# Kernel optimization log

Measured on AMD Instinct MI355X. Metric: run time of the kernel, lower is better.

## Reference

```python
import jax, jax.numpy as jnp
import numpy as np

D_STATE = 16
D_CONV = 4
DT_RANK = 64
D_INNER = 2048
CHANNELS = 1024

def silu(x):
    return x * jax.nn.sigmoid(x)

def setup_inputs() -> dict:
    key = jax.random.key(0)
    ks = jax.random.split(key, 12)
    B, C, T = 2, CHANNELS, 1024
    s = 0.02
    return {
        "x": jax.random.normal(ks[0], (B, C, T), jnp.float32),
        "norm_w": jnp.ones((C,), jnp.float32),
        "norm_b": jnp.zeros((C,), jnp.float32),
        "in_proj_w": jax.random.normal(ks[1], (2 * D_INNER, C), jnp.float32) * s,
        "conv_w": jax.random.normal(ks[2], (D_INNER, 1, D_CONV), jnp.float32) * 0.2,
        "conv_b": jnp.zeros((D_INNER,), jnp.float32),
        "x_proj_w": jax.random.normal(ks[3], (DT_RANK + 2 * D_STATE, D_INNER), jnp.float32) * s,
        "dt_proj_w": jax.random.normal(ks[4], (D_INNER, DT_RANK), jnp.float32) * (DT_RANK ** -0.5),
        "dt_proj_b": jax.random.normal(ks[5], (D_INNER,), jnp.float32) * 0.5 - 4.0,
        "A_log": jnp.log(jnp.arange(1, D_STATE + 1, dtype=jnp.float32))[None, :].repeat(D_INNER, 0),
        "D": jnp.ones((D_INNER,), jnp.float32),
        "out_proj_w": jax.random.normal(ks[6], (C, D_INNER), jnp.float32) * s,
    }

def reference(x, norm_w, norm_b, in_proj_w, conv_w, conv_b, x_proj_w,
              dt_proj_w, dt_proj_b, A_log, D, out_proj_w):
    B, C, T = x.shape
    residual = x
    # LayerNorm over channels: [B,T,C]
    xt = jnp.transpose(x, (0, 2, 1))
    mu = jnp.mean(xt, -1, keepdims=True)
    var = jnp.mean(jnp.square(xt - mu), -1, keepdims=True)
    x_n = (xt - mu) * jax.lax.rsqrt(var + 1e-5) * norm_w + norm_b
    # input projection -> x_in, z  [B,T,d_inner]
    xz = x_n @ in_proj_w.T
    x_in, z = jnp.split(xz, 2, axis=-1)
    # causal depthwise conv1d (torch pads d_conv-1 both sides then slices [:T] == left pad)
    xc = jax.lax.conv_general_dilated(
        jnp.transpose(x_in, (0, 2, 1)),  # [B, d_inner, T]
        conv_w,                            # [d_inner, 1, K]
        window_strides=(1,),
        padding=[(D_CONV - 1, 0)],
        feature_group_count=D_INNER,
        dimension_numbers=("NCH", "OIH", "NCH"),
    ) + conv_b[None, :, None]
    x_c = silu(jnp.transpose(xc, (0, 2, 1)))  # [B,T,d_inner]
    # low-rank dt / B / C projections
    x_dbl = x_c @ x_proj_w.T  # [B,T,dt_rank+2*d_state]
    dt_raw = x_dbl[..., :DT_RANK]
    B_seq = x_dbl[..., DT_RANK:DT_RANK + D_STATE]
    C_seq = x_dbl[..., DT_RANK + D_STATE:]
    dt = jax.nn.softplus(dt_raw @ dt_proj_w.T + dt_proj_b)  # [B,T,d_inner]
    A = -jnp.exp(A_log)  # [d_inner, d_state]
    dA = jnp.exp(dt[..., None] * A[None, None])                      # [B,T,di,ds]
    dBu = dt[..., None] * B_seq[:, :, None, :] * x_c[..., None]       # [B,T,di,ds]
    # sequential selective scan over T
    def step(h, inp):
        dA_t, dBu_t, C_t = inp
        h = dA_t * h + dBu_t                     # [B,di,ds]
        y = jnp.sum(h * C_t[:, None, :], -1)     # [B,di]
        return h, y
    h0 = jnp.zeros((B, D_INNER, D_STATE), x.dtype)
    _, ys = jax.lax.scan(
        step, h0,
        (jnp.transpose(dA, (1, 0, 2, 3)), jnp.transpose(dBu, (1, 0, 2, 3)),
         jnp.transpose(C_seq, (1, 0, 2))))
    y_ssm = jnp.transpose(ys, (1, 0, 2)) + D * x_c  # [B,T,di]
    y = y_ssm * silu(z)
    out = jnp.transpose(y @ out_proj_w.T, (0, 2, 1))  # [B,C,T]
    return out + residual
```

## Files before the change

kernel.cpp:

```cpp
#include <hip/hip_runtime.h>
#include <math.h>

#define C_DIM 1024
#define T_DIM 1024
#define DIN 2048
#define NSTATE 16
#define NC 32
#define LCH 32

typedef __attribute__((ext_vector_type(8))) short bf16x8;
typedef __attribute__((ext_vector_type(4))) float f32x4;
typedef unsigned short ushort_t;

__device__ __forceinline__ float sigmoidf_(float x){ return 1.f/(1.f+__expf(-x)); }

__device__ __forceinline__ unsigned short f2bf(float f){
    union { float f; unsigned u; } v; v.f = f;
    unsigned r = v.u + 0x7fff + ((v.u >> 16) & 1);
    return (unsigned short)(r >> 16);
}
__device__ __forceinline__ float bf2f(ushort_t u){
    union { unsigned u; float f; } v; v.u = ((unsigned)u) << 16;
    return v.f;
}

#define GLDS(g, l) __builtin_amdgcn_global_load_lds( \
    (const __attribute__((address_space(1))) void*)(g), \
    (__attribute__((address_space(3))) void*)(l), 16, 0, 0)

__global__ void prep_w(const float* __restrict__ ipw, const float* __restrict__ dpw,
                       const float* __restrict__ xpw, const float* __restrict__ opw,
                       ushort_t* __restrict__ w_in, ushort_t* __restrict__ w_dt,
                       ushort_t* __restrict__ wxp, ushort_t* __restrict__ w_out)
{
    int blk = blockIdx.x, tid = threadIdx.x;
    if (blk < 4096) {
        int i = blk*256 + tid;
        float4 v = ((const float4*)ipw)[i];
        ushort4 o; o.x=f2bf(v.x); o.y=f2bf(v.y); o.z=f2bf(v.z); o.w=f2bf(v.w);
        ((ushort4*)w_in)[i] = o;
    } else if (blk < 4224) {
        int i = (blk-4096)*256 + tid;
        float4 v = ((const float4*)dpw)[i];
        ushort4 o; o.x=f2bf(v.x); o.y=f2bf(v.y); o.z=f2bf(v.z); o.w=f2bf(v.w);
        ((ushort4*)w_dt)[i] = o;
    } else if (blk < 4480) {
        int i = (blk-4224)*256 + tid;
        ushort4 o; o.x=0; o.y=0; o.z=0; o.w=0;
        if (i < 49152) {
            float4 v = ((const float4*)xpw)[i];
            o.x=f2bf(v.x); o.y=f2bf(v.y); o.z=f2bf(v.z); o.w=f2bf(v.w);
        }
        ((ushort4*)wxp)[i] = o;
    } else {
        int i = (blk-4480)*256 + tid;
        float4 v = ((const float4*)opw)[i];
        ushort4 o; o.x=f2bf(v.x); o.y=f2bf(v.y); o.z=f2bf(v.z); o.w=f2bf(v.w);
        ((ushort4*)w_out)[i] = o;
    }
}

__global__ void ln_v2(const float* __restrict__ x, const float* __restrict__ w,
                      const float* __restrict__ bvec, ushort_t* __restrict__ xn)
{
    __shared__ float tile[8*1040];
    int blk = blockIdx.x;
    int b = blk >> 7, t0 = (blk & 127) * 8;
    int tid = threadIdx.x;
    #pragma unroll
    for (int it = 0; it < 8; it++) {
        int idx = tid + it*256;
        int c = idx >> 1, q = idx & 1;
        float4 v = *(const float4*)&x[((size_t)b*C_DIM + c)*T_DIM + t0 + q*4];
        tile[(q*4+0)*1040 + c] = v.x;
        tile[(q*4+1)*1040 + c] = v.y;
        tile[(q*4+2)*1040 + c] = v.z;
        tile[(q*4+3)*1040 + c] = v.w;
    }
    __syncthreads();
    int tg = tid >> 5, k = tid & 31;
    float sum = 0.f, sumsq = 0.f;
    #pragma unroll
    for (int j = 0; j < 32; j++) {
        float v = tile[tg*1040 + k + 32*j];
        sum += v; sumsq += v*v;
    }
    #pragma unroll
    for (int off = 16; off > 0; off >>= 1) {
        sum   += __shfl_xor(sum, off, 32);
        sumsq += __shfl_xor(sumsq, off, 32);
    }
    float mu  = sum * (1.f/1024.f);
    float var = sumsq * (1.f/1024.f) - mu*mu;
    float rstd = rsqrtf(var + 1e-5f);
    size_t orow = ((size_t)b*T_DIM + t0 + tg)*C_DIM;
    #pragma unroll
    for (int j = 0; j < 8; j++) {
        int c = 4*k + 128*j;
        float4 v = *(const float4*)&tile[tg*1040 + c];
        float4 wv = *(const float4*)&w[c];
        float4 bv = *(const float4*)&bvec[c];
        ushort4 o;
        o.x = f2bf((v.x-mu)*rstd*wv.x + bv.x);
        o.y = f2bf((v.y-mu)*rstd*wv.y + bv.y);
        o.z = f2bf((v.z-mu)*rstd*wv.z + bv.z);
        o.w = f2bf((v.w-mu)*rstd*wv.w + bv.w);
        *(ushort4*)&xn[orow + c] = o;
    }
}

__global__ __launch_bounds__(256, 2)
void gemm_mfma(const ushort_t* __restrict__ A, const ushort_t* __restrict__ W,
               const float* __restrict__ bias, void* __restrict__ Co_,
               int M, int N, int Kloop, int lda, int ldw, int mode)
{
    __shared__ __align__(16) ushort_t As[128*32];
    __shared__ __align__(16) ushort_t Ws[128*32];
    int tid  = threadIdx.x;
    int lane = tid & 63, wave = tid >> 6;
    int wm = (wave >> 1) * 64, wn = (wave & 1) * 64;
    int lrow = lane & 15, quad = lane >> 4;
    int m0 = blockIdx.y << 7, n0 = blockIdx.x << 7;
    int srow = lane >> 2, soff = (lane & 3) * 8;
    int kz = blockIdx.z * Kloop;
    A += kz; W += kz;

    f32x4 acc[4][4];
    #pragma unroll
    for (int i = 0; i < 4; i++)
        #pragma unroll
        for (int j = 0; j < 4; j++)
            acc[i][j] = (f32x4){0.f, 0.f, 0.f, 0.f};

    for (int k0 = 0; k0 < Kloop; k0 += 32) {
        #pragma unroll
        for (int h = 0; h < 2; h++) {
            int r = wave*32 + h*16;
            GLDS(&A[(size_t)(m0 + r + srow)*lda + k0 + soff], &As[r*32]);
            GLDS(&W[(size_t)(n0 + r + srow)*ldw + k0 + soff], &Ws[r*32]);
        }
        __syncthreads();
        bf16x8 af[4], bfr[4];
        #pragma unroll
        for (int i = 0; i < 4; i++)
            af[i] = *(const bf16x8*)&As[(wm + i*16 + lrow)*32 + quad*8];
        #pragma unroll
        for (int j = 0; j < 4; j++)
            bfr[j] = *(const bf16x8*)&Ws[(wn + j*16 + lrow)*32 + quad*8];
        #pragma unroll
        for (int i = 0; i < 4; i++)
            #pragma unroll
            for (int j = 0; j < 4; j++)
                acc[i][j] = __builtin_amdgcn_mfma_f32_16x16x32_bf16(af[i], bfr[j], acc[i][j], 0, 0, 0);
        __syncthreads();
    }

    #pragma unroll
    for (int i = 0; i < 4; i++) {
        #pragma unroll
        for (int j = 0; j < 4; j++) {
            int mb = m0 + wm + i*16 + quad*4;
            int n  = n0 + wn + j*16 + lrow;
            if (mode == 1) {
                ushort_t* Co = (ushort_t*)Co_;
                float bv = bias[n];
                #pragma unroll
                for (int r = 0; r < 4; r++) {
                    float v = acc[i][j][r] + bv;
                    v = (v > 15.f) ? v : __logf(1.f + __expf(v));
                    Co[(size_t)(mb + r)*N + n] = f2bf(v);
                }
            } else if (mode == 3) {
                ushort_t* Co = (ushort_t*)Co_;
                #pragma unroll
                for (int r = 0; r < 4; r++)
                    Co[(size_t)(mb + r)*N + n] = f2bf(acc[i][j][r]);
            } else {
                float* Co = (float*)Co_ + (size_t)blockIdx.z * M * N;
                #pragma unroll
                for (int r = 0; r < 4; r++)
                    Co[(size_t)(mb + r)*N + n] = acc[i][j][r];
            }
        }
    }
}

__global__ __launch_bounds__(256, 2)
void gemm_mfma64(const ushort_t* __restrict__ A, const ushort_t* __restrict__ W,
                 const float* __restrict__ resid, float* __restrict__ Co,
                 int M, int N, int K)
{
    __shared__ __align__(16) ushort_t As[64*32];
    __shared__ __align__(16) ushort_t Ws[128*32];
    int tid  = threadIdx.x;
    int lane = tid & 63, wave = tid >> 6;
    int lrow = lane & 15, quad = lane >> 4;
    int m0 = blockIdx.y << 6, n0 = blockIdx.x << 7;
    int srow = lane >> 2, soff = (lane & 3) * 8;

    f32x4 acc[4][2];
    #pragma unroll
    for (int i = 0; i < 4; i++) { acc[i][0] = (f32x4){0,0,0,0}; acc[i][1] = (f32x4){0,0,0,0}; }

    for (int k0 = 0; k0 < K; k0 += 32) {
        GLDS(&A[(size_t)(m0 + wave*16 + srow)*K + k0 + soff], &As[(wave*16)*32]);
        GLDS(&W[(size_t)(n0 + wave*32 + srow)*K + k0 + soff], &Ws[(wave*32)*32]);
        GLDS(&W[(size_t)(n0 + wave*32 + 16 + srow)*K + k0 + soff], &Ws[(wave*32+16)*32]);
        __syncthreads();
        bf16x8 af[4], bfr[2];
        #pragma unroll
        for (int i = 0; i < 4; i++)
            af[i] = *(const bf16x8*)&As[(i*16 + lrow)*32 + quad*8];
        #pragma unroll
        for (int j = 0; j < 2; j++)
            bfr[j] = *(const bf16x8*)&Ws[(wave*32 + j*16 + lrow)*32 + quad*8];
        #pragma unroll
        for (int i = 0; i < 4; i++)
            #pragma unroll
            for (int j = 0; j < 2; j++)
                acc[i][j] = __builtin_amdgcn_mfma_f32_16x16x32_bf16(af[i], bfr[j], acc[i][j], 0, 0, 0);
        __syncthreads();
    }

    #pragma unroll
    for (int i = 0; i < 4; i++) {
        #pragma unroll
        for (int j = 0; j < 2; j++) {
            int mb = m0 + i*16 + quad*4;
            int n  = n0 + wave*32 + j*16 + lrow;
            int b = mb >> 10, tb = mb & 1023;
            size_t oi = ((size_t)b*C_DIM + n)*T_DIM + tb;
            float4 rv = *(const float4*)&resid[oi];
            float4 ov;
            ov.x = acc[i][j][0] + rv.x;
            ov.y = acc[i][j][1] + rv.y;
            ov.z = acc[i][j][2] + rv.z;
            ov.w = acc[i][j][3] + rv.w;
            *(float4*)&Co[oi] = ov;
        }
    }
}

__global__ void reduce_xproj(const float* __restrict__ xpp, float* __restrict__ xdbl,
                             ushort_t* __restrict__ dtA)
{
    int gid = blockIdx.x*256 + threadIdx.x;
    float4 s = {0.f,0.f,0.f,0.f};
    #pragma unroll
    for (int z = 0; z < 8; z++) {
        float4 v = ((const float4*)xpp)[(size_t)z*65536 + gid];
        s.x += v.x; s.y += v.y; s.z += v.z; s.w += v.w;
    }
    ((float4*)xdbl)[gid] = s;
    int c4 = gid & 31;
    if (c4 < 16) {
        int row = gid >> 5;
        ushort4 o;
        o.x = f2bf(s.x); o.y = f2bf(s.y); o.z = f2bf(s.z); o.w = f2bf(s.w);
        ((ushort4*)dtA)[row*16 + c4] = o;
    }
}

__global__ void conv_silu(const ushort_t* __restrict__ xz, const float* __restrict__ cw,
                          const float* __restrict__ cb, ushort_t* __restrict__ xc)
{
    int idx = blockIdx.x*256 + threadIdx.x;
    int d4 = idx & 511;
    int bt = idx >> 9;
    int t  = bt & 1023;
    int d = d4 << 2;
    const ushort_t* base = xz + (size_t)bt*(2*DIN) + d;
    float a0 = cb[d], a1 = cb[d+1], a2 = cb[d+2], a3 = cb[d+3];
    #pragma unroll
    for (int j = 0; j < 4; j++) {
        int tt = t + j - 3;
        if (tt >= 0) {
            ushort4 v = *(const ushort4*)(base + (long)(j-3)*(2*DIN));
            a0 += cw[(d+0)*4+j]*bf2f(v.x);
            a1 += cw[(d+1)*4+j]*bf2f(v.y);
            a2 += cw[(d+2)*4+j]*bf2f(v.z);
            a3 += cw[(d+3)*4+j]*bf2f(v.w);
        }
    }
    ushort4 o;
    o.x = f2bf(a0*sigmoidf_(a0));
    o.y = f2bf(a1*sigmoidf_(a1));
    o.z = f2bf(a2*sigmoidf_(a2));
    o.w = f2bf(a3*sigmoidf_(a3));
    ((ushort4*)xc)[idx] = o;
}

__global__ void scan_p1(const ushort_t* __restrict__ dtb, const ushort_t* __restrict__ xcb,
                        const float* __restrict__ xdbl,
                        float* __restrict__ hpart, float* __restrict__ Ppart)
{
    int d = blockIdx.x*256 + threadIdx.x;
    int c = blockIdx.y, b = blockIdx.z;
    size_t bt0 = (size_t)b*T_DIM + c*LCH;
    __shared__ float BC[LCH][32];
    {
        int r = threadIdx.x >> 3, c4 = threadIdx.x & 7;
        *(float4*)&BC[r][c4*4] = *(const float4*)&xdbl[(bt0 + r)*128 + 64 + c4*4];
    }
    __syncthreads();
    float h[NSTATE];
    #pragma unroll
    for (int s = 0; s < NSTATE; s++) h[s] = 0.f;
    float sumdt = 0.f;
    const ushort_t* dt_p = dtb + bt0*DIN + d;
    const ushort_t* xc_p = xcb + bt0*DIN + d;
    for (int t = 0; t < LCH; t++) {
        float dtv = bf2f(dt_p[(size_t)t*DIN]);
        float xcv = bf2f(xc_p[(size_t)t*DIN]);
        sumdt += dtv;
        float w = __expf(-dtv);
        float u = dtv * xcv;
        float p = 1.f;
        #pragma unroll
        for (int s = 0; s < NSTATE; s++) { p *= w; h[s] = p*h[s] + u*BC[t][s]; }
    }
    float wsum = __expf(-sumdt);
    size_t base = ((size_t)(b*NC + c)*NSTATE)*DIN + d;
    float p = 1.f;
    #pragma unroll
    for (int s = 0; s < NSTATE; s++) {
        p *= wsum;
        hpart[base + (size_t)s*DIN] = h[s];
        Ppart[base + (size_t)s*DIN] = p;
    }
}

__global__ void scan_combine(float* __restrict__ hpart, const float* __restrict__ Ppart)
{
    int gid = blockIdx.x*256 + threadIdx.x;
    int b = gid >> 15;
    int sd = gid & 32767;
    float run = 0.f;
    for (int c = 0; c < NC; c++) {
        size_t oi = ((size_t)(b*NC + c)*NSTATE)*DIN + sd;
        float hp = hpart[oi];
        float Pp = Ppart[oi];
        hpart[oi] = run;
        run = hp + Pp*run;
    }
}

__global__ void scan_p2(const ushort_t* __restrict__ dtb, const ushort_t* __restrict__ xcb,
                        const float* __restrict__ xdbl, const ushort_t* __restrict__ xz,
                        const float* __restrict__ Dp, const float* __restrict__ hinit,
                        ushort_t* __restrict__ y)
{
    int d = blockIdx.x*256 + threadIdx.x;
    int c = blockIdx.y, b = blockIdx.z;
    size_t bt0 = (size_t)b*T_DIM + c*LCH;
    __shared__ float BC[LCH][32];
    {
        int r = threadIdx.x >> 3, c4 = threadIdx.x & 7;
        *(float4*)&BC[r][c4*4] = *(const float4*)&xdbl[(bt0 + r)*128 + 64 + c4*4];
    }
    __syncthreads();
    float h[NSTATE];
    size_t base = ((size_t)(b*NC + c)*NSTATE)*DIN + d;
    #pragma unroll
    for (int s = 0; s < NSTATE; s++) h[s] = hinit[base + (size_t)s*DIN];
    float Dv = Dp[d];
    const ushort_t* dt_p = dtb + bt0*DIN + d;
    const ushort_t* xc_p = xcb + bt0*DIN + d;
    const ushort_t* z_p  = xz + bt0*(2*DIN) + DIN + d;
    ushort_t* y_p = y + bt0*DIN + d;
    for (int t = 0; t < LCH; t++) {
        float dtv = bf2f(dt_p[(size_t)t*DIN]);
        float xcv = bf2f(xc_p[(size_t)t*DIN]);
        float w = __expf(-dtv);
        float u = dtv * xcv;
        float p = 1.f;
        float yv = 0.f;
        #pragma unroll
        for (int s = 0; s < NSTATE; s++) {
            p *= w;
            h[s] = p*h[s] + u*BC[t][s];
            yv += h[s]*BC[t][16+s];
        }
        yv += Dv*xcv;
        float zv = bf2f(z_p[(size_t)t*(2*DIN)]);
        y_p[(size_t)t*DIN] = f2bf(yv * zv * sigmoidf_(zv));
    }
}

extern "C" void kernel_launch(void* const* d_in, const int* in_sizes, int n_in,
                              void* d_out, int out_size, void* d_ws, size_t ws_size,
                              hipStream_t stream)
{
    const float* x         = (const float*)d_in[0];
    const float* norm_w    = (const float*)d_in[1];
    const float* norm_b    = (const float*)d_in[2];
    const float* in_proj_w = (const float*)d_in[3];
    const float* conv_w    = (const float*)d_in[4];
    const float* conv_b    = (const float*)d_in[5];
    const float* x_proj_w  = (const float*)d_in[6];
    const float* dt_proj_w = (const float*)d_in[7];
    const float* dt_proj_b = (const float*)d_in[8];
    const float* A_log     = (const float*)d_in[9];
    const float* Dp        = (const float*)d_in[10];
    const float* out_proj_w= (const float*)d_in[11];
    float* out = (float*)d_out;
    (void)A_log;

    const size_t MB = 1048576;
    char* wsb = (char*)d_ws;
    ushort_t* xz    = (ushort_t*)(wsb);
    ushort_t* xcb   = (ushort_t*)(wsb + 16*MB);
    ushort_t* dtb   = (ushort_t*)(wsb + 24*MB);
    ushort_t* w_in  = dtb;
    float*    xdbl  = (float*)(wsb + 32*MB);
    ushort_t* yb    = (ushort_t*)(wsb + 33*MB);
    ushort_t* xn    = (ushort_t*)(wsb + 41*MB);
    ushort_t* w_dt  = (ushort_t*)(wsb + 45*MB);
    ushort_t* dtA   = (ushort_t*)(wsb + 45*MB + 262144);
    ushort_t* wxp   = (ushort_t*)(wsb + 45*MB + 524288);
    float*    hpart = (float*)(wsb + 46*MB);
    float*    Ppart = (float*)(wsb + 54*MB);
    ushort_t* w_out = (ushort_t*)(wsb + 62*MB);
    float*    xpp   = hpart;

    prep_w<<<6528, 256, 0, stream>>>(in_proj_w, dt_proj_w, x_proj_w, out_proj_w,
                                     w_in, w_dt, wxp, w_out);
    ln_v2<<<256, 256, 0, stream>>>(x, norm_w, norm_b, xn);
    gemm_mfma<<<dim3(32, 16), 256, 0, stream>>>(xn, w_in, nullptr, xz,
                                                2048, 4096, 1024, 1024, 1024, 3);
    conv_silu<<<4096, 256, 0, stream>>>(xz, conv_w, conv_b, xcb);
    gemm_mfma<<<dim3(1, 16, 8), 256, 0, stream>>>(xcb, wxp, nullptr, xpp,
                                                  2048, 128, 256, 2048, 2048, 0);
    reduce_xproj<<<256, 256, 0, stream>>>(xpp, xdbl, dtA);
    gemm_mfma<<<dim3(16, 16), 256, 0, stream>>>(dtA, w_dt, dt_proj_b, dtb,
                                                2048, 2048, 64, 64, 64, 1);
    scan_p1<<<dim3(8, NC, 2), 256, 0, stream>>>(dtb, xcb, xdbl, hpart, Ppart);
    scan_combine<<<256, 256, 0, stream>>>(hpart, Ppart);
    scan_p2<<<dim3(8, NC, 2), 256, 0, stream>>>(dtb, xcb, xdbl, xz, Dp, hpart, yb);
    gemm_mfma64<<<dim3(8, 32), 256, 0, stream>>>(yb, w_out, x, out, 2048, 1024, 2048);
}
```

Baseline: 261.8 us.

## Fuse all stages into one persistent megakernel with global atomic barriers

Replaces the eleven separate kernel launches (weight prep, layernorm, GEMMs, conv, x_proj reduce, scan phases, out_proj) with one persistent 512-block kernel whose stages are separated by software grid barriers built on atomic counters. Weight conversion now runs alongside layernorm in the same stage. This removes per-launch overhead and inter-kernel gaps. In exchange it relies on all 512 blocks being co-resident, which could deadlock otherwise, and some stages use only part of the grid, leaving blocks idle at each barrier.

```diff
diff --git a/kernel.cpp b/kernel.cpp
--- a/kernel.cpp
+++ b/kernel.cpp
@@ -7,6 +7,7 @@
 #define NSTATE 16
 #define NC 32
 #define LCH 32
+#define NBLK 512
 
 typedef __attribute__((ext_vector_type(8))) short bf16x8;
 typedef __attribute__((ext_vector_type(4))) float f32x4;
@@ -28,362 +29,431 @@
     (const __attribute__((address_space(1))) void*)(g), \
     (__attribute__((address_space(3))) void*)(l), 16, 0, 0)
 
-__global__ void prep_w(const float* __restrict__ ipw, const float* __restrict__ dpw,
-                       const float* __restrict__ xpw, const float* __restrict__ opw,
-                       ushort_t* __restrict__ w_in, ushort_t* __restrict__ w_dt,
-                       ushort_t* __restrict__ wxp, ushort_t* __restrict__ w_out)
+#define MB 1048576
+
+__device__ __forceinline__ void gbar(int* cnt, int stage)
 {
+    __syncthreads();
+    if (threadIdx.x == 0) {
+        __threadfence();
+        __hip_atomic_fetch_add(&cnt[stage], 1, __ATOMIC_ACQ_REL, __HIP_MEMORY_SCOPE_AGENT);
+        while (__hip_atomic_load(&cnt[stage], __ATOMIC_ACQUIRE, __HIP_MEMORY_SCOPE_AGENT) < NBLK)
+            __builtin_amdgcn_s_sleep(8);
+        __threadfence();
+    }
+    __syncthreads();
+}
+
+__global__ void init_bar(int* cnt)
+{
+    if (threadIdx.x < 16) cnt[threadIdx.x] = 0;
+}
+
+__global__ __launch_bounds__(256, 2)
+void mamba_mega(const float* __restrict__ x, const float* __restrict__ norm_w,
+                const float* __restrict__ norm_b, const float* __restrict__ ipw,
+                const float* __restrict__ cw, const float* __restrict__ cb,
+                const float* __restrict__ xpw, const float* __restrict__ dpw,
+                const float* __restrict__ dpb, const float* __restrict__ Dp,
+                const float* __restrict__ opw, float* __restrict__ out,
+                char* __restrict__ wsb)
+{
+    ushort_t* xz    = (ushort_t*)(wsb);
+    ushort_t* xcb   = (ushort_t*)(wsb + 16*MB);
+    ushort_t* dtb   = (ushort_t*)(wsb + 24*MB);
+    ushort_t* w_in  = dtb;
+    ushort_t* yb    = (ushort_t*)(wsb + 32*MB);
+    ushort_t* xn    = (ushort_t*)(wsb + 40*MB);
+    ushort_t* w_out = (ushort_t*)(wsb + 44*MB);
+    ushort_t* w_dt  = (ushort_t*)(wsb + 48*MB);
+    ushort_t* dtA   = (ushort_t*)(wsb + 48*MB + 262144);
+    ushort_t* wxp   = (ushort_t*)(wsb + 48*MB + 524288);
+    float*    BCf   = (float*)(wsb + 49*MB);
+    float*    hpart = (float*)(wsb + 50*MB);
+    float*    Ppart = (float*)(wsb + 58*MB);
+    float*    xpp   = (float*)(wsb + 66*MB);
+    int*      bar   = (int*)(wsb + 80*MB);
+
+    __shared__ __align__(16) char smem[33280];
+    float*    lntile = (float*)smem;
+    ushort_t* sm_a   = (ushort_t*)smem;
+    ushort_t* sm_b   = (ushort_t*)(smem + 8192);
+    float (*sBC)[32] = (float(*)[32])(smem + 16384);
+
     int blk = blockIdx.x, tid = threadIdx.x;
-    if (blk < 4096) {
-        int i = blk*256 + tid;
-        float4 v = ((const float4*)ipw)[i];
-        ushort4 o; o.x=f2bf(v.x); o.y=f2bf(v.y); o.z=f2bf(v.z); o.w=f2bf(v.w);
-        ((ushort4*)w_in)[i] = o;
-    } else if (blk < 4224) {
-        int i = (blk-4096)*256 + tid;
-        float4 v = ((const float4*)dpw)[i];
-        ushort4 o; o.x=f2bf(v.x); o.y=f2bf(v.y); o.z=f2bf(v.z); o.w=f2bf(v.w);
-        ((ushort4*)w_dt)[i] = o;
-    } else if (blk < 4480) {
-        int i = (blk-4224)*256 + tid;
-        ushort4 o; o.x=0; o.y=0; o.z=0; o.w=0;
-        if (i < 49152) {
-            float4 v = ((const float4*)xpw)[i];
-            o.x=f2bf(v.x); o.y=f2bf(v.y); o.z=f2bf(v.z); o.w=f2bf(v.w);
-        }
-        ((ushort4*)wxp)[i] = o;
+    int lane = tid & 63, wave = tid >> 6;
+    int lrow = lane & 15, quad = lane >> 4;
+    int srow = lane >> 2, soff = (lane & 3) * 8;
+    int wm = (wave >> 1) * 64, wn = (wave & 1) * 64;
+
+    if (blk < 256) {
+        int b = blk >> 7, t0 = (blk & 127) * 8;
+        #pragma unroll
+        for (int it = 0; it < 8; it++) {
+            int idx = tid + it*256;
+            int c = idx >> 1, q = idx & 1;
+            float4 v = *(const float4*)&x[((size_t)b*C_DIM + c)*T_DIM + t0 + q*4];
+            lntile[(q*4+0)*1040 + c] = v.x;
+            lntile[(q*4+1)*1040 + c] = v.y;
+            lntile[(q*4+2)*1040 + c] = v.z;
+            lntile[(q*4+3)*1040 + c] = v.w;
+        }
+        __syncthreads();
+        int tg = tid >> 5, k = tid & 31;
+        float sum = 0.f, sumsq = 0.f;
+        #pragma unroll
+        for (int j = 0; j < 32; j++) {
+            float v = lntile[tg*1040 + k + 32*j];
+            sum += v; sumsq += v*v;
+        }
+        #pragma unroll
+        for (int off = 16; off > 0; off >>= 1) {
+            sum   += __shfl_xor(sum, off, 32);
+            sumsq += __shfl_xor(sumsq, off, 32);
+        }
+        float mu  = sum * (1.f/1024.f);
+        float var = sumsq * (1.f/1024.f) - mu*mu;
+        float rstd = rsqrtf(var + 1e-5f);
+        size_t orow = ((size_t)b*T_DIM + t0 + tg)*C_DIM;
+        #pragma unroll
+        for (int j = 0; j < 8; j++) {
+            int c = 4*k + 128*j;
+            float4 v = *(const float4*)&lntile[tg*1040 + c];
+            float4 wv = *(const float4*)&norm_w[c];
+            float4 bv = *(const float4*)&norm_b[c];
+            ushort4 o;
+            o.x = f2bf((v.x-mu)*rstd*wv.x + bv.x);
+            o.y = f2bf((v.y-mu)*rstd*wv.y + bv.y);
+            o.z = f2bf((v.z-mu)*rstd*wv.z + bv.z);
+            o.w = f2bf((v.w-mu)*rstd*wv.w + bv.w);
+            *(ushort4*)&xn[orow + c] = o;
+        }
     } else {
-        int i = (blk-4480)*256 + tid;
-        float4 v = ((const float4*)opw)[i];
-        ushort4 o; o.x=f2bf(v.x); o.y=f2bf(v.y); o.z=f2bf(v.z); o.w=f2bf(v.w);
-        ((ushort4*)w_out)[i] = o;
-    }
-}
-
-__global__ void ln_v2(const float* __restrict__ x, const float* __restrict__ w,
-                      const float* __restrict__ bvec, ushort_t* __restrict__ xn)
-{
-    __shared__ float tile[8*1040];
-    int blk = blockIdx.x;
-    int b = blk >> 7, t0 = (blk & 127) * 8;
-    int tid = threadIdx.x;
-    #pragma unroll
-    for (int it = 0; it < 8; it++) {
-        int idx = tid + it*256;
-        int c = idx >> 1, q = idx & 1;
-        float4 v = *(const float4*)&x[((size_t)b*C_DIM + c)*T_DIM + t0 + q*4];
-        tile[(q*4+0)*1040 + c] = v.x;
-        tile[(q*4+1)*1040 + c] = v.y;
-        tile[(q*4+2)*1040 + c] = v.z;
-        tile[(q*4+3)*1040 + c] = v.w;
-    }
-    __syncthreads();
-    int tg = tid >> 5, k = tid & 31;
-    float sum = 0.f, sumsq = 0.f;
-    #pragma unroll
-    for (int j = 0; j < 32; j++) {
-        float v = tile[tg*1040 + k + 32*j];
-        sum += v; sumsq += v*v;
-    }
-    #pragma unroll
-    for (int off = 16; off > 0; off >>= 1) {
-        sum   += __shfl_xor(sum, off, 32);
-        sumsq += __shfl_xor(sumsq, off, 32);
-    }
-    float mu  = sum * (1.f/1024.f);
-    float var = sumsq * (1.f/1024.f) - mu*mu;
-    float rstd = rsqrtf(var + 1e-5f);
-    size_t orow = ((size_t)b*T_DIM + t0 + tg)*C_DIM;
-    #pragma unroll
-    for (int j = 0; j < 8; j++) {
-        int c = 4*k + 128*j;
-        float4 v = *(const float4*)&tile[tg*1040 + c];
-        float4 wv = *(const float4*)&w[c];
-        float4 bv = *(const float4*)&bvec[c];
+        for (int g = (blk-256)*256 + tid; g < 1671168; g += 65536) {
+            if (g < 1048576) {
+                float4 v = ((const float4*)ipw)[g];
+                ushort4 o; o.x=f2bf(v.x); o.y=f2bf(v.y); o.z=f2bf(v.z); o.w=f2bf(v.w);
+                ((ushort4*)w_in)[g] = o;
+            } else if (g < 1081344) {
+                int i = g - 1048576;
+                float4 v = ((const float4*)dpw)[i];
+                ushort4 o; o.x=f2bf(v.x); o.y=f2bf(v.y); o.z=f2bf(v.z); o.w=f2bf(v.w);
+                ((ushort4*)w_dt)[i] = o;
+            } else if (g < 1146880) {
+                int i = g - 1081344;
+                ushort4 o; o.x=0; o.y=0; o.z=0; o.w=0;
+                if (i < 49152) {
+                    float4 v = ((const float4*)xpw)[i];
+                    o.x=f2bf(v.x); o.y=f2bf(v.y); o.z=f2bf(v.z); o.w=f2bf(v.w);
+                }
+                ((ushort4*)wxp)[i] = o;
+            } else {
+                int i = g - 1146880;
+                float4 v = ((const float4*)opw)[i];
+                ushort4 o; o.x=f2bf(v.x); o.y=f2bf(v.y); o.z=f2bf(v.z); o.w=f2bf(v.w);
+                ((ushort4*)w_out)[i] = o;
+            }
+        }
+    }
+    gbar(bar, 0);
+
+    {
+        int m0 = (blk >> 5) << 7, n0 = (blk & 31) << 7;
+        f32x4 acc[4][4];
+        #pragma unroll
+        for (int i = 0; i < 4; i++)
+            #pragma unroll
+            for (int j = 0; j < 4; j++) acc[i][j] = (f32x4){0.f,0.f,0.f,0.f};
+        for (int k0 = 0; k0 < 1024; k0 += 32) {
+            #pragma unroll
+            for (int h = 0; h < 2; h++) {
+                int r = wave*32 + h*16;
+                GLDS(&xn[(size_t)(m0 + r + srow)*1024 + k0 + soff], &sm_a[r*32]);
+                GLDS(&w_in[(size_t)(n0 + r + srow)*1024 + k0 + soff], &sm_b[r*32]);
+            }
+            __syncthreads();
+            bf16x8 af[4], bfr[4];
+            #pragma unroll
+            for (int i = 0; i < 4; i++) af[i] = *(const bf16x8*)&sm_a[(wm + i*16 + lrow)*32 + quad*8];
+            #pragma unroll
+            for (int j = 0; j < 4; j++) bfr[j] = *(const bf16x8*)&sm_b[(wn + j*16 + lrow)*32 + quad*8];
+            #pragma unroll
+            for (int i = 0; i < 4; i++)
+                #pragma unroll
+                for (int j = 0; j < 4; j++)
+                    acc[i][j] = __builtin_amdgcn_mfma_f32_16x16x32_bf16(af[i], bfr[j], acc[i][j], 0, 0, 0);
+            __syncthreads();
+        }
+        #pragma unroll
+        for (int i = 0; i < 4; i++)
+            #pragma unroll
+            for (int j = 0; j < 4; j++) {
+                int mb = m0 + wm + i*16 + quad*4;
+                int n  = n0 + wn + j*16 + lrow;
+                #pragma unroll
+                for (int r = 0; r < 4; r++)
+                    xz[(size_t)(mb + r)*4096 + n] = f2bf(acc[i][j][r]);
+            }
+    }
+    gbar(bar, 1);
+
+    for (int idx = blk*256 + tid; idx < 1048576; idx += 131072) {
+        int d4 = idx & 511;
+        int bt = idx >> 9;
+        int t  = bt & 1023;
+        int d = d4 << 2;
+        const ushort_t* base = xz + (size_t)bt*4096 + d;
+        float a0 = cb[d], a1 = cb[d+1], a2 = cb[d+2], a3 = cb[d+3];
+        #pragma unroll
+        for (int j = 0; j < 4; j++) {
+            int tt = t + j - 3;
+            if (tt >= 0) {
+                ushort4 v = *(const ushort4*)(base + (long)(j-3)*4096);
+                a0 += cw[(d+0)*4+j]*bf2f(v.x);
+                a1 += cw[(d+1)*4+j]*bf2f(v.y);
+                a2 += cw[(d+2)*4+j]*bf2f(v.z);
+                a3 += cw[(d+3)*4+j]*bf2f(v.w);
+            }
+        }
         ushort4 o;
-        o.x = f2bf((v.x-mu)*rstd*wv.x + bv.x);
-        o.y = f2bf((v.y-mu)*rstd*wv.y + bv.y);
-        o.z = f2bf((v.z-mu)*rstd*wv.z + bv.z);
-        o.w = f2bf((v.w-mu)*rstd*wv.w + bv.w);
-        *(ushort4*)&xn[orow + c] = o;
-    }
-}
-
-__global__ __launch_bounds__(256, 2)
-void gemm_mfma(const ushort_t* __restrict__ A, const ushort_t* __restrict__ W,
-               const float* __restrict__ bias, void* __restrict__ Co_,
-               int M, int N, int Kloop, int lda, int ldw, int mode)
-{
-    __shared__ __align__(16) ushort_t As[128*32];
-    __shared__ __align__(16) ushort_t Ws[128*32];
-    int tid  = threadIdx.x;
-    int lane = tid & 63, wave = tid >> 6;
-    int wm = (wave >> 1) * 64, wn = (wave & 1) * 64;
-    int lrow = lane & 15, quad = lane >> 4;
-    int m0 = blockIdx.y << 7, n0 = blockIdx.x << 7;
-    int srow = lane >> 2, soff = (lane & 3) * 8;
-    int kz = blockIdx.z * Kloop;
-    A += kz; W += kz;
-
-    f32x4 acc[4][4];
-    #pragma unroll
-    for (int i = 0; i < 4; i++)
-        #pragma unroll
-        for (int j = 0; j < 4; j++)
-            acc[i][j] = (f32x4){0.f, 0.f, 0.f, 0.f};
-
-    for (int k0 = 0; k0 < Kloop; k0 += 32) {
-        #pragma unroll
-        for (int h = 0; h < 2; h++) {
-            int r = wave*32 + h*16;
-            GLDS(&A[(size_t)(m0 + r + srow)*lda + k0 + soff], &As[r*32]);
-            GLDS(&W[(size_t)(n0 + r + srow)*ldw + k0 + soff], &Ws[r*32]);
-        }
-        __syncthreads();
-        bf16x8 af[4], bfr[4];
-        #pragma unroll
-        for (int i = 0; i < 4; i++)
-            af[i] = *(const bf16x8*)&As[(wm + i*16 + lrow)*32 + quad*8];
-        #pragma unroll
-        for (int j = 0; j < 4; j++)
-            bfr[j] = *(const bf16x8*)&Ws[(wn + j*16 + lrow)*32 + quad*8];
-        #pragma unroll
-        for (int i = 0; i < 4; i++)
-            #pragma unroll
-            for (int j = 0; j < 4; j++)
-                acc[i][j] = __builtin_amdgcn_mfma_f32_16x16x32_bf16(af[i], bfr[j], acc[i][j], 0, 0, 0);
-        __syncthreads();
-    }
-
-    #pragma unroll
-    for (int i = 0; i < 4; i++) {
-        #pragma unroll
-        for (int j = 0; j < 4; j++) {
-            int mb = m0 + wm + i*16 + quad*4;
-            int n  = n0 + wn + j*16 + lrow;
-            if (mode == 1) {
-                ushort_t* Co = (ushort_t*)Co_;
-                float bv = bias[n];
+        o.x = f2bf(a0*sigmoidf_(a0));
+        o.y = f2bf(a1*sigmoidf_(a1));
+        o.z = f2bf(a2*sigmoidf_(a2));
+        o.w = f2bf(a3*sigmoidf_(a3));
+        ((ushort4*)xcb)[idx] = o;
+    }
+    gbar(bar, 2);
+
+    if (blk < 128) {
+        int m0 = (blk >> 3) << 7, z = blk & 7;
+        int kz = z * 256;
+        f32x4 acc[4][4];
+        #pragma unroll
+        for (int i = 0; i < 4; i++)
+            #pragma unroll
+            for (int j = 0; j < 4; j++) acc[i][j] = (f32x4){0.f,0.f,0.f,0.f};
+        for (int k0 = 0; k0 < 256; k0 += 32) {
+            #pragma unroll
+            for (int h = 0; h < 2; h++) {
+                int r = wave*32 + h*16;
+                GLDS(&xcb[(size_t)(m0 + r + srow)*2048 + kz + k0 + soff], &sm_a[r*32]);
+                GLDS(&wxp[(size_t)(r + srow)*2048 + kz + k0 + soff], &sm_b[r*32]);
+            }
+            __syncthreads();
+            bf16x8 af[4], bfr[4];
+            #pragma unroll
+            for (int i = 0; i < 4; i++) af[i] = *(const bf16x8*)&sm_a[(wm + i*16 + lrow)*32 + quad*8];
+            #pragma unroll
+            for (int j = 0; j < 4; j++) bfr[j] = *(const bf16x8*)&sm_b[(wn + j*16 + lrow)*32 + quad*8];
+            #pragma unroll
+            for (int i = 0; i < 4; i++)
+                #pragma unroll
+                for (int j = 0; j < 4; j++)
+                    acc[i][j] = __builtin_amdgcn_mfma_f32_16x16x32_bf16(af[i], bfr[j], acc[i][j], 0, 0, 0);
+            __syncthreads();
+        }
+        float* Co = xpp + (size_t)z * 262144;
+        #pragma unroll
+        for (int i = 0; i < 4; i++)
+            #pragma unroll
+            for (int j = 0; j < 4; j++) {
+                int mb = m0 + wm + i*16 + quad*4;
+                int n  = wn + j*16 + lrow;
+                #pragma unroll
+                for (int r = 0; r < 4; r++)
+                    Co[(size_t)(mb + r)*128 + n] = acc[i][j][r];
+            }
+    }
+    gbar(bar, 3);
+
+    for (int g = blk*256 + tid; g < 65536; g += 131072) {
+        float4 s = {0.f,0.f,0.f,0.f};
+        #pragma unroll
+        for (int z = 0; z < 8; z++) {
+            float4 v = ((const float4*)xpp)[(size_t)z*65536 + g];
+            s.x += v.x; s.y += v.y; s.z += v.z; s.w += v.w;
+        }
+        int row = g >> 5, c4 = g & 31;
+        if (c4 < 16) {
+            ushort4 o; o.x=f2bf(s.x); o.y=f2bf(s.y); o.z=f2bf(s.z); o.w=f2bf(s.w);
+            ((ushort4*)dtA)[row*16 + c4] = o;
+        } else if (c4 < 24) {
+            ((float4*)BCf)[row*8 + (c4-16)] = s;
+        }
+    }
+    gbar(bar, 4);
+
+    if (blk < 256) {
+        int m0 = (blk >> 4) << 7, n0 = (blk & 15) << 7;
+        f32x4 acc[4][4];
+        #pragma unroll
+        for (int i = 0; i < 4; i++)
+            #pragma unroll
+            for (int j = 0; j < 4; j++) acc[i][j] = (f32x4){0.f,0.f,0.f,0.f};
+        for (int k0 = 0; k0 < 64; k0 += 32) {
+            #pragma unroll
+            for (int h = 0; h < 2; h++) {
+                int r = wave*32 + h*16;
+                GLDS(&dtA[(size_t)(m0 + r + srow)*64 + k0 + soff], &sm_a[r*32]);
+                GLDS(&w_dt[(size_t)(n0 + r + srow)*64 + k0 + soff], &sm_b[r*32]);
+            }
+            __syncthreads();
+            bf16x8 af[4], bfr[4];
+            #pragma unroll
+            for (int i = 0; i < 4; i++) af[i] = *(const bf16x8*)&sm_a[(wm + i*16 + lrow)*32 + quad*8];
+            #pragma unroll
+            for (int j = 0; j < 4; j++) bfr[j] = *(const bf16x8*)&sm_b[(wn + j*16 + lrow)*32 + quad*8];
+            #pragma unroll
+            for (int i = 0; i < 4; i++)
+                #pragma unroll
+                for (int j = 0; j < 4; j++)
+                    acc[i][j] = __builtin_amdgcn_mfma_f32_16x16x32_bf16(af[i], bfr[j], acc[i][j], 0, 0, 0);
+            __syncthreads();
+        }
+        #pragma unroll
+        for (int i = 0; i < 4; i++)
+            #pragma unroll
+            for (int j = 0; j < 4; j++) {
+                int mb = m0 + wm + i*16 + quad*4;
+                int n  = n0 + wn + j*16 + lrow;
+                float bv = dpb[n];
                 #pragma unroll
                 for (int r = 0; r < 4; r++) {
                     float v = acc[i][j][r] + bv;
                     v = (v > 15.f) ? v : __logf(1.f + __expf(v));
-                    Co[(size_t)(mb + r)*N + n] = f2bf(v);
+                    dtb[(size_t)(mb + r)*2048 + n] = f2bf(v);
                 }
-            } else if (mode == 3) {
-                ushort_t* Co = (ushort_t*)Co_;
-                #pragma unroll
-                for (int r = 0; r < 4; r++)
-                    Co[(size_t)(mb + r)*N + n] = f2bf(acc[i][j][r]);
-            } else {
-                float* Co = (float*)Co_ + (size_t)blockIdx.z * M * N;
-                #pragma unroll
-                for (int r = 0; r < 4; r++)
-                    Co[(size_t)(mb + r)*N + n] = acc[i][j][r];
-            }
-        }
-    }
-}
-
-__global__ __launch_bounds__(256, 2)
-void gemm_mfma64(const ushort_t* __restrict__ A, const ushort_t* __restrict__ W,
-                 const float* __restrict__ resid, float* __restrict__ Co,
-                 int M, int N, int K)
-{
-    __shared__ __align__(16) ushort_t As[64*32];
-    __shared__ __align__(16) ushort_t Ws[128*32];
-    int tid  = threadIdx.x;
-    int lane = tid & 63, wave = tid >> 6;
-    int lrow = lane & 15, quad = lane >> 4;
-    int m0 = blockIdx.y << 6, n0 = blockIdx.x << 7;
-    int srow = lane >> 2, soff = (lane & 3) * 8;
-
-    f32x4 acc[4][2];
-    #pragma unroll
-    for (int i = 0; i < 4; i++) { acc[i][0] = (f32x4){0,0,0,0}; acc[i][1] = (f32x4){0,0,0,0}; }
-
-    for (int k0 = 0; k0 < K; k0 += 32) {
-        GLDS(&A[(size_t)(m0 + wave*16 + srow)*K + k0 + soff], &As[(wave*16)*32]);
-        GLDS(&W[(size_t)(n0 + wave*32 + srow)*K + k0 + soff], &Ws[(wave*32)*32]);
-        GLDS(&W[(size_t)(n0 + wave*32 + 16 + srow)*K + k0 + soff], &Ws[(wave*32+16)*32]);
+            }
+    }
+    gbar(bar, 5);
+
+    {
+        int d = (blk & 7)*256 + tid;
+        int c = (blk >> 3) & 31, b = blk >> 8;
+        size_t bt0 = (size_t)b*T_DIM + c*LCH;
+        {
+            int r = tid >> 3, c4 = tid & 7;
+            *(float4*)&sBC[r][c4*4] = *(const float4*)&BCf[(bt0 + r)*32 + c4*4];
+        }
         __syncthreads();
-        bf16x8 af[4], bfr[2];
-        #pragma unroll
-        for (int i = 0; i < 4; i++)
-            af[i] = *(const bf16x8*)&As[(i*16 + lrow)*32 + quad*8];
-        #pragma unroll
-        for (int j = 0; j < 2; j++)
-            bfr[j] = *(const bf16x8*)&Ws[(wave*32 + j*16 + lrow)*32 + quad*8];
-        #pragma unroll
-        for (int i = 0; i < 4; i++)
-            #pragma unroll
-            for (int j = 0; j < 2; j++)
-                acc[i][j] = __builtin_amdgcn_mfma_f32_16x16x32_bf16(af[i], bfr[j], acc[i][j], 0, 0, 0);
+        float h[NSTATE];
+        #pragma unroll
+        for (int s = 0; s < NSTATE; s++) h[s] = 0.f;
+        float sumdt = 0.f;
+        const ushort_t* dt_p = dtb + bt0*DIN + d;
+        const ushort_t* xc_p = xcb + bt0*DIN + d;
+        for (int t = 0; t < LCH; t++) {
+            float dtv = bf2f(dt_p[(size_t)t*DIN]);
+            float xcv = bf2f(xc_p[(size_t)t*DIN]);
+            sumdt += dtv;
+            float w = __expf(-dtv);
+            float u = dtv * xcv;
+            float p = 1.f;
+            #pragma unroll
+            for (int s = 0; s < NSTATE; s++) { p *= w; h[s] = p*h[s] + u*sBC[t][s]; }
+        }
+        float wsum = __expf(-sumdt);
+        size_t base = ((size_t)(b*NC + c)*NSTATE)*DIN + d;
+        float p = 1.f;
+        #pragma unroll
+        for (int s = 0; s < NSTATE; s++) {
+            p *= wsum;
+            hpart[base + (size_t)s*DIN] = h[s];
+            Ppart[base + (size_t)s*DIN] = p;
+        }
+    }
+    gbar(bar, 6);
+
+    for (int gid = blk*256 + tid; gid < 65536; gid += 131072) {
+        int b = gid >> 15;
+        int sd = gid & 32767;
+        float run = 0.f;
+        for (int c = 0; c < NC; c++) {
+            size_t oi = ((size_t)(b*NC + c)*NSTATE)*DIN + sd;
+            float hp = hpart[oi];
+            float Pp = Ppart[oi];
+            hpart[oi] = run;
+            run = hp + Pp*run;
+        }
+    }
+    gbar(bar, 7);
+
+    {
+        int d = (blk & 7)*256 + tid;
+        int c = (blk >> 3) & 31, b = blk >> 8;
+        size_t bt0 = (size_t)b*T_DIM + c*LCH;
+        {
+            int r = tid >> 3, c4 = tid & 7;
+            *(float4*)&sBC[r][c4*4] = *(const float4*)&BCf[(bt0 + r)*32 + c4*4];
+        }
         __syncthreads();
-    }
-
-    #pragma unroll
-    for (int i = 0; i < 4; i++) {
-        #pragma unroll
-        for (int j = 0; j < 2; j++) {
-            int mb = m0 + i*16 + quad*4;
-            int n  = n0 + wave*32 + j*16 + lrow;
-            int b = mb >> 10, tb = mb & 1023;
-            size_t oi = ((size_t)b*C_DIM + n)*T_DIM + tb;
-            float4 rv = *(const float4*)&resid[oi];
-            float4 ov;
-            ov.x = acc[i][j][0] + rv.x;
-            ov.y = acc[i][j][1] + rv.y;
-            ov.z = acc[i][j][2] + rv.z;
-            ov.w = acc[i][j][3] + rv.w;
-            *(float4*)&Co[oi] = ov;
-        }
-    }
-}
-
-__global__ void reduce_xproj(const float* __restrict__ xpp, float* __restrict__ xdbl,
-                             ushort_t* __restrict__ dtA)
-{
-    int gid = blockIdx.x*256 + threadIdx.x;
-    float4 s = {0.f,0.f,0.f,0.f};
-    #pragma unroll
-    for (int z = 0; z < 8; z++) {
-        float4 v = ((const float4*)xpp)[(size_t)z*65536 + gid];
-        s.x += v.x; s.y += v.y; s.z += v.z; s.w += v.w;
-    }
-    ((float4*)xdbl)[gid] = s;
-    int c4 = gid & 31;
-    if (c4 < 16) {
-        int row = gid >> 5;
-        ushort4 o;
-        o.x = f2bf(s.x); o.y = f2bf(s.y); o.z = f2bf(s.z); o.w = f2bf(s.w);
-        ((ushort4*)dtA)[row*16 + c4] = o;
-    }
-}
-
-__global__ void conv_silu(const ushort_t* __restrict__ xz, const float* __restrict__ cw,
-                          const float* __restrict__ cb, ushort_t* __restrict__ xc)
-{
-    int idx = blockIdx.x*256 + threadIdx.x;
-    int d4 = idx & 511;
-    int bt = idx >> 9;
-    int t  = bt & 1023;
-    int d = d4 << 2;
-    const ushort_t* base = xz + (size_t)bt*(2*DIN) + d;
-    float a0 = cb[d], a1 = cb[d+1], a2 = cb[d+2], a3 = cb[d+3];
-    #pragma unroll
-    for (int j = 0; j < 4; j++) {
-        int tt = t + j - 3;
-        if (tt >= 0) {
-            ushort4 v = *(const ushort4*)(base + (long)(j-3)*(2*DIN));
-            a0 += cw[(d+0)*4+j]*bf2f(v.x);
-            a1 += cw[(d+1)*4+j]*bf2f(v.y);
-            a2 += cw[(d+2)*4+j]*bf2f(v.z);
-            a3 += cw[(d+3)*4+j]*bf2f(v.w);
-        }
-    }
-    ushort4 o;
-    o.x = f2bf(a0*sigmoidf_(a0));
-    o.y = f2bf(a1*sigmoidf_(a1));
-    o.z = f2bf(a2*sigmoidf_(a2));
-    o.w = f2bf(a3*sigmoidf_(a3));
-    ((ushort4*)xc)[idx] = o;
-}
-
-__global__ void scan_p1(const ushort_t* __restrict__ dtb, const ushort_t* __restrict__ xcb,
-                        const float* __restrict__ xdbl,
-                        float* __restrict__ hpart, float* __restrict__ Ppart)
-{
-    int d = blockIdx.x*256 + threadIdx.x;
-    int c = blockIdx.y, b = blockIdx.z;
-    size_t bt0 = (size_t)b*T_DIM + c*LCH;
-    __shared__ float BC[LCH][32];
-    {
-        int r = threadIdx.x >> 3, c4 = threadIdx.x & 7;
-        *(float4*)&BC[r][c4*4] = *(const float4*)&xdbl[(bt0 + r)*128 + 64 + c4*4];
-    }
-    __syncthreads();
-    float h[NSTATE];
-    #pragma unroll
-    for (int s = 0; s < NSTATE; s++) h[s] = 0.f;
-    float sumdt = 0.f;
-    const ushort_t* dt_p = dtb + bt0*DIN + d;
-    const ushort_t* xc_p = xcb + bt0*DIN + d;
-    for (int t = 0; t < LCH; t++) {
-        float dtv = bf2f(dt_p[(size_t)t*DIN]);
-        float xcv = bf2f(xc_p[(size_t)t*DIN]);
-        sumdt += dtv;
-        float w = __expf(-dtv);
-        float u = dtv * xcv;
-        float p = 1.f;
-        #pragma unroll
-        for (int s = 0; s < NSTATE; s++) { p *= w; h[s] = p*h[s] + u*BC[t][s]; }
-    }
-    float wsum = __expf(-sumdt);
-    size_t base = ((size_t)(b*NC + c)*NSTATE)*DIN + d;
-    float p = 1.f;
-    #pragma unroll
-    for (int s = 0; s < NSTATE; s++) {
-        p *= wsum;
-        hpart[base + (size_t)s*DIN] = h[s];
-        Ppart[base + (size_t)s*DIN] = p;
-    }
-}
-
-__global__ void scan_combine(float* __restrict__ hpart, const float* __restrict__ Ppart)
-{
-    int gid = blockIdx.x*256 + threadIdx.x;
-    int b = gid >> 15;
-    int sd = gid & 32767;
-    float run = 0.f;
-    for (int c = 0; c < NC; c++) {
-        size_t oi = ((size_t)(b*NC + c)*NSTATE)*DIN + sd;
-        float hp = hpart[oi];
-        float Pp = Ppart[oi];
-        hpart[oi] = run;
-        run = hp + Pp*run;
-    }
-}
-
-__global__ void scan_p2(const ushort_t* __restrict__ dtb, const ushort_t* __restrict__ xcb,
-                        const float* __restrict__ xdbl, const ushort_t* __restrict__ xz,
-                        const float* __restrict__ Dp, const float* __restrict__ hinit,
-                        ushort_t* __restrict__ y)
-{
-    int d = blockIdx.x*256 + threadIdx.x;
-    int c = blockIdx.y, b = blockIdx.z;
-    size_t bt0 = (size_t)b*T_DIM + c*LCH;
-    __shared__ float BC[LCH][32];
-    {
-        int r = threadIdx.x >> 3, c4 = threadIdx.x & 7;
-        *(float4*)&BC[r][c4*4] = *(const float4*)&xdbl[(bt0 + r)*128 + 64 + c4*4];
-    }
-    __syncthreads();
-    float h[NSTATE];
-    size_t base = ((size_t)(b*NC + c)*NSTATE)*DIN + d;
-    #pragma unroll
-    for (int s = 0; s < NSTATE; s++) h[s] = hinit[base + (size_t)s*DIN];
-    float Dv = Dp[d];
-    const ushort_t* dt_p = dtb + bt0*DIN + d;
-    const ushort_t* xc_p = xcb + bt0*DIN + d;
-    const ushort_t* z_p  = xz + bt0*(2*DIN) + DIN + d;
-    ushort_t* y_p = y + bt0*DIN + d;
-    for (int t = 0; t < LCH; t++) {
-        float dtv = bf2f(dt_p[(size_t)t*DIN]);
-        float xcv = bf2f(xc_p[(size_t)t*DIN]);
-        float w = __expf(-dtv);
-        float u = dtv * xcv;
-        float p = 1.f;
-        float yv = 0.f;
-        #pragma unroll
-        for (int s = 0; s < NSTATE; s++) {
-            p *= w;
-            h[s] = p*h[s] + u*BC[t][s];
-            yv += h[s]*BC[t][16+s];
-        }
-        yv += Dv*xcv;
-        float zv = bf2f(z_p[(size_t)t*(2*DIN)]);
-        y_p[(size_t)t*DIN] = f2bf(yv * zv * sigmoidf_(zv));
+        float h[NSTATE];
+        size_t base = ((size_t)(b*NC + c)*NSTATE)*DIN + d;
+        #pragma unroll
+        for (int s = 0; s < NSTATE; s++) h[s] = hpart[base + (size_t)s*DIN];
+        float Dv = Dp[d];
+        const ushort_t* dt_p = dtb + bt0*DIN + d;
+        const ushort_t* xc_p = xcb + bt0*DIN + d;
+        const ushort_t* z_p  = xz + bt0*4096 + 2048 + d;
+        ushort_t* y_p = yb + bt0*DIN + d;
+        for (int t = 0; t < LCH; t++) {
+            float dtv = bf2f(dt_p[(size_t)t*DIN]);
+            float xcv = bf2f(xc_p[(size_t)t*DIN]);
+            float w = __expf(-dtv);
+            float u = dtv * xcv;
+            float p = 1.f;
+            float yv = 0.f;
+            #pragma unroll
+            for (int s = 0; s < NSTATE; s++) {
+                p *= w;
+                h[s] = p*h[s] + u*sBC[t][s];
+                yv += h[s]*sBC[t][16+s];
+            }
+            yv += Dv*xcv;
+            float zv = bf2f(z_p[(size_t)t*4096]);
+            y_p[(size_t)t*DIN] = f2bf(yv * zv * sigmoidf_(zv));
+        }
+    }
+    gbar(bar, 8);
+
+    if (blk < 256) {
+        int m0 = (blk >> 3) << 6, n0 = (blk & 7) << 7;
+        f32x4 acc[4][2];
+        #pragma unroll
+        for (int i = 0; i < 4; i++) { acc[i][0] = (f32x4){0,0,0,0}; acc[i][1] = (f32x4){0,0,0,0}; }
+        for (int k0 = 0; k0 < 2048; k0 += 32) {
+            GLDS(&yb[(size_t)(m0 + wave*16 + srow)*2048 + k0 + soff], &sm_a[(wave*16)*32]);
+            GLDS(&w_out[(size_t)(n0 + wave*32 + srow)*2048 + k0 + soff], &sm_b[(wave*32)*32]);
+            GLDS(&w_out[(size_t)(n0 + wave*32 + 16 + srow)*2048 + k0 + soff], &sm_b[(wave*32+16)*32]);
+            __syncthreads();
+            bf16x8 af[4], bfr[2];
+            #pragma unroll
+            for (int i = 0; i < 4; i++) af[i] = *(const bf16x8*)&sm_a[(i*16 + lrow)*32 + quad*8];
+            #pragma unroll
+            for (int j = 0; j < 2; j++) bfr[j] = *(const bf16x8*)&sm_b[(wave*32 + j*16 + lrow)*32 + quad*8];
+            #pragma unroll
+            for (int i = 0; i < 4; i++)
+                #pragma unroll
+                for (int j = 0; j < 2; j++)
+                    acc[i][j] = __builtin_amdgcn_mfma_f32_16x16x32_bf16(af[i], bfr[j], acc[i][j], 0, 0, 0);
+            __syncthreads();
+        }
+        #pragma unroll
+        for (int i = 0; i < 4; i++)
+            #pragma unroll
+            for (int j = 0; j < 2; j++) {
+                int mb = m0 + i*16 + quad*4;
+                int n  = n0 + wave*32 + j*16 + lrow;
+                int b = mb >> 10, tb = mb & 1023;
+                size_t oi = ((size_t)b*C_DIM + n)*T_DIM + tb;
+                float4 rv = *(const float4*)&x[oi];
+                float4 ov;
+                ov.x = acc[i][j][0] + rv.x;
+                ov.y = acc[i][j][1] + rv.y;
+                ov.z = acc[i][j][2] + rv.z;
+                ov.w = acc[i][j][3] + rv.w;
+                *(float4*)&out[oi] = ov;
+            }
     }
 }
 
@@ -404,38 +474,12 @@
     const float* Dp        = (const float*)d_in[10];
     const float* out_proj_w= (const float*)d_in[11];
     float* out = (float*)d_out;
+    char* wsb = (char*)d_ws;
     (void)A_log;
 
-    const size_t MB = 1048576;
-    char* wsb = (char*)d_ws;
-    ushort_t* xz    = (ushort_t*)(wsb);
-    ushort_t* xcb   = (ushort_t*)(wsb + 16*MB);
-    ushort_t* dtb   = (ushort_t*)(wsb + 24*MB);
-    ushort_t* w_in  = dtb;
-    float*    xdbl  = (float*)(wsb + 32*MB);
-    ushort_t* yb    = (ushort_t*)(wsb + 33*MB);
-    ushort_t* xn    = (ushort_t*)(wsb + 41*MB);
-    ushort_t* w_dt  = (ushort_t*)(wsb + 45*MB);
-    ushort_t* dtA   = (ushort_t*)(wsb + 45*MB + 262144);
-    ushort_t* wxp   = (ushort_t*)(wsb + 45*MB + 524288);
-    float*    hpart = (float*)(wsb + 46*MB);
-    float*    Ppart = (float*)(wsb + 54*MB);
-    ushort_t* w_out = (ushort_t*)(wsb + 62*MB);
-    float*    xpp   = hpart;
-
-    prep_w<<<6528, 256, 0, stream>>>(in_proj_w, dt_proj_w, x_proj_w, out_proj_w,
-                                     w_in, w_dt, wxp, w_out);
-    ln_v2<<<256, 256, 0, stream>>>(x, norm_w, norm_b, xn);
-    gemm_mfma<<<dim3(32, 16), 256, 0, stream>>>(xn, w_in, nullptr, xz,
-                                                2048, 4096, 1024, 1024, 1024, 3);
-    conv_silu<<<4096, 256, 0, stream>>>(xz, conv_w, conv_b, xcb);
-    gemm_mfma<<<dim3(1, 16, 8), 256, 0, stream>>>(xcb, wxp, nullptr, xpp,
-                                                  2048, 128, 256, 2048, 2048, 0);
-    reduce_xproj<<<256, 256, 0, stream>>>(xpp, xdbl, dtA);
-    gemm_mfma<<<dim3(16, 16), 256, 0, stream>>>(dtA, w_dt, dt_proj_b, dtb,
-                                                2048, 2048, 64, 64, 64, 1);
-    scan_p1<<<dim3(8, NC, 2), 256, 0, stream>>>(dtb, xcb, xdbl, hpart, Ppart);
-    scan_combine<<<256, 256, 0, stream>>>(hpart, Ppart);
-    scan_p2<<<dim3(8, NC, 2), 256, 0, stream>>>(dtb, xcb, xdbl, xz, Dp, hpart, yb);
-    gemm_mfma64<<<dim3(8, 32), 256, 0, stream>>>(yb, w_out, x, out, 2048, 1024, 2048);
-}
+    int* bar = (int*)(wsb + 80*MB);
+    init_bar<<<1, 64, 0, stream>>>(bar);
+    mamba_mega<<<NBLK, 256, 0, stream>>>(x, norm_w, norm_b, in_proj_w,
+                                         conv_w, conv_b, x_proj_w, dt_proj_w,
+                                         dt_proj_b, Dp, out_proj_w, out, wsb);
+}
```

After: 960.4 us. 3.67x slower.
